# Optimization experiments

Measured on AMD Instinct MI355X. Metric: run time of the kernel, lower is better.

Reference implementation:

```python
import jax, jax.numpy as jnp
import numpy as np

N = 100000
E = 1600000
IN_C = 128
HID = 256
EPS = 1e-5


def setup_inputs() -> dict:
    key = jax.random.key(0)
    ks = jax.random.split(key, 20)
    s = lambda fi, fo: (1.0 / np.sqrt(fi))
    inp = {
        "x": jax.random.normal(ks[0], (N, IN_C), dtype=jnp.float32),
        "edge_index": jax.random.randint(ks[1], (2, E), 0, N, dtype=jnp.int64),
        # SAGEConv (in -> hidden): lin_l (on aggregated neighbors, with bias), lin_r (root, no bias)
        "Wl": jax.random.normal(ks[2], (HID, IN_C), dtype=jnp.float32) * s(IN_C, HID),
        "bl": jnp.zeros((HID,), dtype=jnp.float32),
        "Wr": jax.random.normal(ks[3], (HID, IN_C), dtype=jnp.float32) * s(IN_C, HID),
        # bns[0]
        "bn_g": jnp.ones((HID,), dtype=jnp.float32),
        "bn_b": jnp.zeros((HID,), dtype=jnp.float32),
        # linear stack hidden->hidden->64->14->2
        "W1": jax.random.normal(ks[4], (HID, HID), dtype=jnp.float32) * s(HID, HID),
        "b1": jnp.zeros((HID,), dtype=jnp.float32),
        "W2": jax.random.normal(ks[5], (64, HID), dtype=jnp.float32) * s(HID, 64),
        "b2": jnp.zeros((64,), dtype=jnp.float32),
        "W3": jax.random.normal(ks[6], (14, 64), dtype=jnp.float32) * s(64, 14),
        "b3": jnp.zeros((14,), dtype=jnp.float32),
        "W4": jax.random.normal(ks[7], (2, 14), dtype=jnp.float32) * s(14, 2),
        "b4": jnp.zeros((2,), dtype=jnp.float32),
        # bns2: BN(hidden), BN(64), BN(14)
        "g1": jnp.ones((HID,), dtype=jnp.float32), "bb1": jnp.zeros((HID,), dtype=jnp.float32),
        "g2": jnp.ones((64,), dtype=jnp.float32), "bb2": jnp.zeros((64,), dtype=jnp.float32),
        "g3": jnp.ones((14,), dtype=jnp.float32), "bb3": jnp.zeros((14,), dtype=jnp.float32),
    }
    return inp


def _bn(h, g, b):
    # training-mode BatchNorm1d: batch mean, biased variance
    m = h.mean(axis=0)
    v = jnp.mean((h - m) ** 2, axis=0)
    return g * (h - m) * jax.lax.rsqrt(v + EPS) + b


def _sage_mean(x, edge_index, Wl, bl, Wr):
    src, dst = edge_index[0], edge_index[1]
    n = x.shape[0]
    agg = jax.ops.segment_sum(x[src], dst, num_segments=n)  # [N, F]
    cnt = jax.ops.segment_sum(jnp.ones((src.shape[0],), x.dtype), dst, num_segments=n)
    agg = agg / jnp.maximum(cnt, 1.0)[:, None]
    return agg @ Wl.T + bl + x @ Wr.T


def reference(x, edge_index, Wl, bl, Wr, bn_g, bn_b,
              W1, b1, W2, b2, W3, b3, W4, b4,
              g1, bb1, g2, bb2, g3, bb3):
    # convs2[:-1] loop (num_layers=2 -> single conv), dropout is identity (eval)
    h = _sage_mean(x, edge_index, Wl, bl, Wr)
    h = jax.nn.relu(_bn(h, bn_g, bn_b))
    # linear stack with bns2 + relu
    h = jax.nn.relu(_bn(h @ W1.T + b1, g1, bb1))
    h = jax.nn.relu(_bn(h @ W2.T + b2, g2, bb2))
    h = jax.nn.relu(_bn(h @ W3.T + b3, g3, bb3))
    h = h @ W4.T + b4
    return jax.nn.log_softmax(h, axis=-1)
```

## Files before the change

### kernel.cpp

```cpp
#include <hip/hip_runtime.h>
#include <math.h>

#define BN_EPS 1e-5f
#define STAT_NB 64
#define GBIN 512
#define BSH 7

typedef unsigned short u16;
typedef __attribute__((ext_vector_type(8))) unsigned short u16x8;
typedef __attribute__((ext_vector_type(8))) short bf16x8;
typedef __attribute__((ext_vector_type(4))) float f32x4;

__device__ __forceinline__ float bf2f(u16 b){
  union{unsigned int u; float f;} c; c.u = ((unsigned int)b)<<16; return c.f;
}
__device__ __forceinline__ u16 f2bf(float f){
  union{float f; unsigned int u;} c; c.f=f;
  unsigned int u = c.u;
  return (u16)((u + 0x7fffu + ((u>>16)&1u)) >> 16);
}

__global__ __launch_bounds__(256) void k_prep(
    const float* __restrict__ Wl, const float* __restrict__ Wr,
    const float* __restrict__ W1, const float* __restrict__ W2,
    const float* __restrict__ x,
    u16* __restrict__ Wb1, u16* __restrict__ Wb2, u16* __restrict__ Wb3,
    u16* __restrict__ Acat, int n, int* __restrict__ flags){
  int bid = blockIdx.x, tid = threadIdx.x;
  if (bid==0 && tid<8) flags[tid]=0;
  auto cv8 = [](const float* s)->u16x8{
    float4 a = ((const float4*)s)[0], b = ((const float4*)s)[1];
    u16x8 v;
    v[0]=f2bf(a.x); v[1]=f2bf(a.y); v[2]=f2bf(a.z); v[3]=f2bf(a.w);
    v[4]=f2bf(b.x); v[5]=f2bf(b.y); v[6]=f2bf(b.z); v[7]=f2bf(b.w);
    return v;
  };
  if (bid < 32){
    int i = bid*256 + tid;
    int c = i>>5, kb = (i&31)*8;
    const float* src = (kb<128) ? (Wl + (size_t)c*128 + kb) : (Wr + (size_t)c*128 + kb-128);
    *(u16x8*)(Wb1 + (size_t)c*256 + kb) = cv8(src);
  } else if (bid < 64){
    int i = (bid-32)*256 + tid;
    *(u16x8*)(Wb2 + (size_t)i*8) = cv8(W1 + (size_t)i*8);
  } else if (bid < 72){
    int i = (bid-64)*256 + tid;
    if (i < 2048) *(u16x8*)(Wb3 + (size_t)i*8) = cv8(W2 + (size_t)i*8);
  } else {
    int i = (bid-72)*256 + tid;
    int total = n*16;
    int stride = (gridDim.x-72)*256;
    for (; i<total; i+=stride){
      int r = i>>4, kb = (i&15)*8;
      *(u16x8*)(Acat + (size_t)r*256 + 128 + kb) = cv8(x + (size_t)r*128 + kb);
    }
  }
}


__global__ __launch_bounds__(256) void k_hist(const int* __restrict__ ei, int E, int nbkt,
                                              int* __restrict__ blkhist){
  __shared__ int hist[1024];
  int tid = threadIdx.x, blk = blockIdx.x;
  for (int b=tid;b<1024;b+=256) hist[b]=0;
  __syncthreads();
  int per = (E + GBIN - 1)/GBIN;
  int e0 = blk*per, e1 = min(E, e0+per);
  for (int e=e0+tid; e<e1; e+=256)
    atomicAdd(&hist[ei[(size_t)E+e]>>BSH], 1);
  __syncthreads();
  for (int b=tid;b<nbkt;b+=256) blkhist[(size_t)b*GBIN + blk] = hist[b];
}

__global__ __launch_bounds__(256) void k_rowscan(int* __restrict__ blkhist, int nbkt,
                                                 int* __restrict__ bbase){
  int wid = (blockIdx.x*blockDim.x + threadIdx.x) >> 6;
  int lane = threadIdx.x & 63;
  if (wid >= nbkt) return;
  int* row = blkhist + (size_t)wid*GBIN + lane*8;
  int v[8];
  #pragma unroll
  for (int j=0;j<8;j++) v[j] = row[j];
  int s = 0;
  #pragma unroll
  for (int j=0;j<8;j++){ int t = v[j]; v[j] = s; s += t; }
  int incl = s;
  #pragma unroll
  for (int o=1;o<64;o<<=1){
    int t = __shfl_up(incl, o, 64);
    if (lane >= o) incl += t;
  }
  int excl = incl - s;
  #pragma unroll
  for (int j=0;j<8;j++) row[j] = v[j] + excl;
  if (lane == 63) bbase[wid] = incl;
}

__global__ void k_bscan(int* __restrict__ bbase, int nbkt){
  __shared__ int s[1024];
  int tid = threadIdx.x;
  int v = (tid<nbkt)? bbase[tid] : 0;
  s[tid]=v; __syncthreads();
  #pragma unroll
  for (int o=1;o<1024;o<<=1){
    int t = (tid>=o)? s[tid-o] : 0;
    __syncthreads();
    s[tid]+=t;
    __syncthreads();
  }
  if (tid<nbkt) bbase[tid] = s[tid]-v;
  if (tid==1023) bbase[nbkt] = s[1023];
}

__global__ __launch_bounds__(256) void k_scatter(const int* __restrict__ ei, int E, int nbkt,
                                                 const int* __restrict__ blkhist,
                                                 const int* __restrict__ bbase,
                                                 int* __restrict__ pairs){
  __shared__ int cur[1024];
  int tid = threadIdx.x, blk = blockIdx.x;
  for (int b=tid;b<nbkt;b+=256) cur[b] = bbase[b] + blkhist[(size_t)b*GBIN + blk];
  __syncthreads();
  int per = (E + GBIN - 1)/GBIN;
  int e0 = blk*per, e1 = min(E, e0+per);
  for (int e=e0+tid; e<e1; e+=256){
    int dst = ei[(size_t)E+e];
    int src = ei[e];
    int b = dst>>BSH;
    int p = atomicAdd(&cur[b], 1);
    pairs[p] = (src<<BSH) | (dst & 127);
  }
}

__global__ __launch_bounds__(256) void k_bucket_csr(const int* __restrict__ pairs,
                                                    const int* __restrict__ bbase,
                                                    int nbkt, int n,
                                                    int* __restrict__ deg, int* __restrict__ off,
                                                    int* __restrict__ eidx){
  __shared__ int hist[128], loff[128], cur2[128];
  int tid = threadIdx.x, b = blockIdx.x;
  if (b >= nbkt) return;
  int n0 = b<<BSH;
  int nn = min(128, n - n0);
  int e0 = bbase[b], e1 = bbase[b+1];
  int cnt = e1 - e0;
  if (tid<128) hist[tid]=0;
  __syncthreads();
  for (int i=tid;i<cnt;i+=256)
    atomicAdd(&hist[pairs[e0+i] & 127], 1);
  __syncthreads();
  int hv=0;
  if (tid<128){ hv = hist[tid]; loff[tid] = hv; }
  __syncthreads();
  #pragma unroll
  for (int o=1;o<128;o<<=1){
    int t = (tid<128 && tid>=o)? loff[tid-o] : 0;
    __syncthreads();
    if (tid<128) loff[tid]+=t;
    __syncthreads();
  }
  if (tid<128){
    int ex = loff[tid]-hv;
    cur2[tid] = ex;
    if (tid<nn){
      deg[n0+tid] = hv;
      off[n0+tid] = e0 + ex;
    }
  }
  __syncthreads();
  for (int i=tid;i<cnt;i+=256){
    int v = pairs[e0+i];
    int p = atomicAdd(&cur2[v & 127], 1);
    eidx[e0 + p] = v>>BSH;
  }
}

__global__ void k_aggregate(u16* Acat, const int* __restrict__ off,
                            const int* __restrict__ deg, const int* __restrict__ eidx, int n){
  int wid = (blockIdx.x*blockDim.x + threadIdx.x) >> 6;
  int lane = threadIdx.x & 63;
  if (wid >= n) return;
  int o = off[wid], d = deg[wid];
  int eslot = lane >> 3;
  int ck = (lane & 7) * 16;
  float f[16];
  #pragma unroll
  for (int j=0;j<16;j++) f[j]=0.f;
  #pragma unroll 2
  for (int i = eslot; i < d; i += 8){
    int s = eidx[o+i];
    const u16x8* src = (const u16x8*)(Acat + (size_t)s*256 + 128 + ck);
    u16x8 v0 = src[0], v1 = src[1];
    #pragma unroll
    for (int j=0;j<8;j++) f[j]   += bf2f(v0[j]);
    #pragma unroll
    for (int j=0;j<8;j++) f[8+j] += bf2f(v1[j]);
  }
  #pragma unroll
  for (int j=0;j<16;j++){
    f[j] += __shfl_xor(f[j], 8, 64);
    f[j] += __shfl_xor(f[j], 16, 64);
    f[j] += __shfl_xor(f[j], 32, 64);
  }
  if (lane < 8){
    float inv = 1.f/(float)max(d,1);
    u16x8 r0, r1;
    #pragma unroll
    for (int j=0;j<8;j++){ r0[j]=f2bf(f[j]*inv); r1[j]=f2bf(f[8+j]*inv); }
    u16x8* dst = (u16x8*)(Acat + (size_t)wid*256 + ck);
    dst[0]=r0; dst[1]=r1;
  }
}


template<int COLS>
__global__ __launch_bounds__(256, 2) void k_gemm_mfma(
    const u16* __restrict__ A, const u16* __restrict__ W,
    const float* __restrict__ ss, int has_ss,
    const float* __restrict__ bias, u16* __restrict__ out,
    int nrows, int hout,
    float* __restrict__ psum, float* __restrict__ psq)
{
  constexpr int WN  = COLS/2;
  constexpr int NFR = WN/16;
  __shared__ u16 As[128*64];
  __shared__ u16 Bs[COLS*64];
  __shared__ float scs[256], shs[256];
  __shared__ float red[2][2][COLS];

  int tid  = threadIdx.x;
  int lane = tid & 63, wave = tid >> 6;
  int wr = wave >> 1, wc = wave & 1;
  int rbase = blockIdx.x*128;
  constexpr int cbase = 0;

  if (has_ss){ scs[tid] = ss[tid]; shs[tid] = ss[256+tid]; }
  __syncthreads();

  f32x4 acc[4][NFR];
  #pragma unroll
  for (int m=0;m<4;m++)
    #pragma unroll
    for (int n=0;n<NFR;n++)
      acc[m][n] = (f32x4){0.f,0.f,0.f,0.f};

  int arow = tid >> 1;
  int acb  = (tid & 1) * 32;
  bool avalid = (rbase + arow) < nrows;
  const u16* aptr = A + (size_t)(rbase+arow)*256 + acb;
  int brow, bcb;
  if (COLS==256)      { brow = tid;    bcb = 0; }
  else if (COLS==128) { brow = tid>>1; bcb = (tid&1)*32; }
  else                { brow = tid>>2; bcb = (tid&3)*16; }
  const u16* bptr = W + (size_t)(cbase+brow)*256 + bcb;

  for (int kt=0; kt<256; kt+=64){
    #pragma unroll
    for (int q=0;q<4;q++){
      u16x8 v = (u16x8){0,0,0,0,0,0,0,0};
      if (avalid) v = *(const u16x8*)(aptr + kt + q*8);
      if (has_ss){
        int k = acb + q*8;
        #pragma unroll
        for (int e=0;e<8;e++){
          float f = bf2f(v[e]);
          f = fmaxf(fmaf(f, scs[kt+k+e], shs[kt+k+e]), 0.f);
          v[e] = f2bf(f);
        }
      }
      int slot = ((acb>>3) + q) ^ (arow & 7);
      *(u16x8*)(As + arow*64 + slot*8) = v;
    }
    #pragma unroll
    for (int q=0;q<(COLS==256?8:COLS/32);q++){
      u16x8 v = *(const u16x8*)(bptr + kt + q*8);
      int slot = ((bcb>>3) + q) ^ (brow & 7);
      *(u16x8*)(Bs + brow*64 + slot*8) = v;
    }
    __syncthreads();

    int fr = lane & 15, g = lane >> 4;
    #pragma unroll
    for (int kk=0;kk<2;kk++){
      bf16x8 af[4], bfr[NFR];
      #pragma unroll
      for (int m=0;m<4;m++){
        int row = wr*64 + m*16 + fr;
        int slot = (kk*4 + g) ^ (row & 7);
        af[m] = *(const bf16x8*)(As + row*64 + slot*8);
      }
      #pragma unroll
      for (int n=0;n<NFR;n++){
        int row = wc*WN + n*16 + fr;
        int slot = (kk*4 + g) ^ (row & 7);
        bfr[n] = *(const bf16x8*)(Bs + row*64 + slot*8);
      }
      #pragma unroll
      for (int m=0;m<4;m++)
        #pragma unroll
        for (int n=0;n<NFR;n++)
          acc[m][n] = __builtin_amdgcn_mfma_f32_16x16x32_bf16(af[m], bfr[n], acc[m][n], 0, 0, 0);
    }
    __syncthreads();
  }

  int cl = lane & 15, g = lane >> 4;
  float bv[NFR], sn[NFR], qn[NFR];
  #pragma unroll
  for (int n=0;n<NFR;n++){
    bv[n] = bias[cbase + wc*WN + n*16 + cl];
    sn[n] = 0.f; qn[n] = 0.f;
  }
  #pragma unroll
  for (int m=0;m<4;m++){
    int r0 = rbase + wr*64 + m*16 + g*4;
    #pragma unroll
    for (int n=0;n<NFR;n++){
      int c = cbase + wc*WN + n*16 + cl;
      #pragma unroll
      for (int i=0;i<4;i++){
        int r = r0 + i;
        if (r < nrows){
          float v = acc[m][n][i] + bv[n];
          out[(size_t)r*hout + c] = f2bf(v);
          sn[n] += v; qn[n] += v*v;
        }
      }
    }
  }
  #pragma unroll
  for (int n=0;n<NFR;n++){
    sn[n] += __shfl_xor(sn[n], 16, 64);
    sn[n] += __shfl_xor(sn[n], 32, 64);
    qn[n] += __shfl_xor(qn[n], 16, 64);
    qn[n] += __shfl_xor(qn[n], 32, 64);
  }
  if (lane < 16){
    #pragma unroll
    for (int n=0;n<NFR;n++){
      int cc = wc*WN + n*16 + lane;
      red[0][wr][cc] = sn[n];
      red[1][wr][cc] = qn[n];
    }
  }
  __syncthreads();
  if (tid < COLS){
    psum[(size_t)blockIdx.x*hout + cbase + tid] = red[0][0][tid] + red[0][1][tid];
    psq [(size_t)blockIdx.x*hout + cbase + tid] = red[1][0][tid] + red[1][1][tid];
  }
}

__global__ __launch_bounds__(256) void k_stats_partfold(
    const float* __restrict__ psum, const float* __restrict__ psq,
    int rt, int h, float* __restrict__ part, float ninv,
    const float* __restrict__ g, const float* __restrict__ b_,
    float* __restrict__ ss, int* __restrict__ counter){
  __shared__ int isLast;
  int c = threadIdx.x, b = blockIdx.x;
  int chunk = (rt + STAT_NB - 1)/STAT_NB;
  int i0 = b*chunk;
  int i1 = min(rt, i0+chunk);
  if (c < h){
    float s0=0.f,s1=0.f,s2=0.f,s3=0.f, q0=0.f,q1=0.f,q2=0.f,q3=0.f;
    int i=i0;
    for (; i+3<i1; i+=4){
      s0 += psum[(size_t)i*h+c];     q0 += psq[(size_t)i*h+c];
      s1 += psum[(size_t)(i+1)*h+c]; q1 += psq[(size_t)(i+1)*h+c];
      s2 += psum[(size_t)(i+2)*h+c]; q2 += psq[(size_t)(i+2)*h+c];
      s3 += psum[(size_t)(i+3)*h+c]; q3 += psq[(size_t)(i+3)*h+c];
    }
    for (; i<i1; ++i){ s0 += psum[(size_t)i*h+c]; q0 += psq[(size_t)i*h+c]; }
    part[((size_t)b*2  )*h + c] = (s0+s1)+(s2+s3);
    part[((size_t)b*2+1)*h + c] = (q0+q1)+(q2+q3);
  }
  __threadfence();
  if (c==0) isLast = (atomicAdd(counter,1) == gridDim.x-1);
  __syncthreads();
  if (isLast && c < h){
    float S0=0.f,S1=0.f,Q0=0.f,Q1=0.f;
    #pragma unroll 2
    for (int b2=0;b2<STAT_NB;b2+=2){
      S0 += part[((size_t)b2*2  )*h + c];
      Q0 += part[((size_t)b2*2+1)*h + c];
      S1 += part[((size_t)(b2+1)*2  )*h + c];
      Q1 += part[((size_t)(b2+1)*2+1)*h + c];
    }
    float S = S0+S1, Q = Q0+Q1;
    float m = S*ninv;
    float v = fmaxf(Q*ninv - m*m, 0.f);
    float sc = g[c] * rsqrtf(v + BN_EPS);
    ss[c]   = sc;
    ss[h+c] = b_[c] - m*sc;
  }
}

__global__ __launch_bounds__(256) void k_lin3(const u16* __restrict__ h3, const float* __restrict__ ss3,
     const float* __restrict__ W3, const float* __restrict__ b3,
     float* __restrict__ h4, int n, float* __restrict__ psum, float* __restrict__ psq){
  __shared__ float Ws[14*64];
  __shared__ float bs[14];
  __shared__ float sc[64], sh[64];
  __shared__ float redp[2][14][4];
  int tid=threadIdx.x;
  for (int i=tid;i<896;i+=256) Ws[i]=W3[i];
  if (tid<14) bs[tid]=b3[tid];
  if (tid<64){ sc[tid]=ss3[tid]; sh[tid]=ss3[64+tid]; }
  __syncthreads();
  int node = blockIdx.x*256 + tid;
  float o[14];
  #pragma unroll
  for (int hh=0;hh<14;hh++) o[hh]=0.f;
  if (node<n){
    const u16x8* ar = (const u16x8*)(h3 + (size_t)node*64);
    #pragma unroll
    for (int kv=0;kv<8;kv++){
      u16x8 v = ar[kv];
      #pragma unroll
      for (int j=0;j<8;j++){
        int k=kv*8+j;
        float a = fmaxf(fmaf(bf2f(v[j]), sc[k], sh[k]), 0.f);
        #pragma unroll
        for (int hh=0;hh<14;hh++) o[hh] = fmaf(a, Ws[hh*64+k], o[hh]);
      }
    }
    #pragma unroll
    for (int hh=0;hh<14;hh++){ o[hh]+=bs[hh]; h4[(size_t)node*14+hh]=o[hh]; }
  }
  int lane = tid & 63, w = tid>>6;
  #pragma unroll
  for (int hh=0;hh<14;hh++){
    float sv = (node<n)? o[hh] : 0.f;
    float qv = sv*sv;
    #pragma unroll
    for (int offs=32;offs>0;offs>>=1){
      sv += __shfl_down(sv,offs,64);
      qv += __shfl_down(qv,offs,64);
    }
    if (lane==0){ redp[0][hh][w]=sv; redp[1][hh][w]=qv; }
  }
  __syncthreads();
  if (tid<14){
    float t=redp[0][tid][0]+redp[0][tid][1]+redp[0][tid][2]+redp[0][tid][3];
    psum[(size_t)blockIdx.x*14+tid]=t;
  } else if (tid>=64 && tid<78){
    int c=tid-64;
    float t=redp[1][c][0]+redp[1][c][1]+redp[1][c][2]+redp[1][c][3];
    psq[(size_t)blockIdx.x*14+c]=t;
  }
}

__global__ void k_final(const float* __restrict__ h4, const float* __restrict__ ss4,
   const float* __restrict__ W4, const float* __restrict__ b4, float* __restrict__ out, int n){
  int node = blockIdx.x*blockDim.x+threadIdx.x;
  if (node>=n) return;
  float z0=b4[0], z1=b4[1];
  #pragma unroll
  for (int j=0;j<14;j++){
    float a = fmaxf(h4[(size_t)node*14+j]*ss4[j]+ss4[14+j], 0.f);
    z0 = fmaf(a, W4[j],    z0);
    z1 = fmaf(a, W4[14+j], z1);
  }
  float m = fmaxf(z0,z1);
  float lse = m + logf(expf(z0-m)+expf(z1-m));
  out[(size_t)node*2]   = z0-lse;
  out[(size_t)node*2+1] = z1-lse;
}

extern "C" void kernel_launch(void* const* d_in, const int* in_sizes, int n_in,
                              void* d_out, int out_size, void* d_ws, size_t ws_size,
                              hipStream_t stream){
  const float* x    = (const float*)d_in[0];
  const int*   ei   = (const int*)d_in[1];
  const float* Wl   = (const float*)d_in[2];
  const float* bl   = (const float*)d_in[3];
  const float* Wr   = (const float*)d_in[4];
  const float* bn_g = (const float*)d_in[5];
  const float* bn_b = (const float*)d_in[6];
  const float* W1   = (const float*)d_in[7];
  const float* b1   = (const float*)d_in[8];
  const float* W2   = (const float*)d_in[9];
  const float* b2   = (const float*)d_in[10];
  const float* W3   = (const float*)d_in[11];
  const float* b3   = (const float*)d_in[12];
  const float* W4   = (const float*)d_in[13];
  const float* b4   = (const float*)d_in[14];
  const float* g1   = (const float*)d_in[15];
  const float* bb1  = (const float*)d_in[16];
  const float* g2   = (const float*)d_in[17];
  const float* bb2  = (const float*)d_in[18];
  const float* g3   = (const float*)d_in[19];
  const float* bb3  = (const float*)d_in[20];

  const int N = in_sizes[0]/128;
  const int E = in_sizes[1]/2;
  const int NBKT = (N + 127) >> BSH;
  const int RT2 = (N+127)/128;
  const int RT4 = (N+255)/256;

  char* p = (char*)d_ws;
  auto alloc = [&](size_t bytes)->void*{
    void* r = (void*)p;
    p += (bytes + 255) & ~(size_t)255;
    return r;
  };
  int* deg      = (int*)alloc((size_t)N*sizeof(int));
  int* off      = (int*)alloc((size_t)N*sizeof(int));
  int* bbase    = (int*)alloc(1025*sizeof(int));
  int* flags    = (int*)alloc(16*sizeof(int));
  int* blkhist  = (int*)alloc((size_t)1024*GBIN*sizeof(int));
  int* pairs    = (int*)alloc((size_t)E*sizeof(int));
  int* eidx     = (int*)alloc((size_t)E*sizeof(int));
  u16* Acat     = (u16*)alloc((size_t)N*256*sizeof(u16));
  u16* h1b      = (u16*)alloc((size_t)N*256*sizeof(u16));
  float* h4     = (float*)alloc((size_t)N*14*sizeof(float));
  u16* Wb1      = (u16*)alloc(256*256*sizeof(u16));
  u16* Wb2      = (u16*)alloc(256*256*sizeof(u16));
  u16* Wb3      = (u16*)alloc(64*256*sizeof(u16));
  float* psum   = (float*)alloc((size_t)RT2*256*sizeof(float));
  float* psq    = (float*)alloc((size_t)RT2*256*sizeof(float));
  float* part   = (float*)alloc((size_t)STAT_NB*2*256*sizeof(float));
  float* ssb    = (float*)alloc(4*512*sizeof(float));
  u16* h2b = Acat;
  u16* h3b = h1b;
  float* ss1=ssb, *ss2=ssb+512, *ss3=ssb+1024, *ss4=ssb+1536;
  const float ninv = 1.f/(float)N;

  k_prep<<<dim3(72+2048), dim3(256), 0, stream>>>(Wl, Wr, W1, W2, x, Wb1, Wb2, Wb3, Acat, N, flags);

  k_hist<<<dim3(GBIN), dim3(256), 0, stream>>>(ei, E, NBKT, blkhist);
  k_rowscan<<<dim3((NBKT*64+255)/256), dim3(256), 0, stream>>>(blkhist, NBKT, bbase);
  k_bscan<<<dim3(1), dim3(1024), 0, stream>>>(bbase, NBKT);
  k_scatter<<<dim3(GBIN), dim3(256), 0, stream>>>(ei, E, NBKT, blkhist, bbase, pairs);
  k_bucket_csr<<<dim3(NBKT), dim3(256), 0, stream>>>(pairs, bbase, NBKT, N, deg, off, eidx);

  k_aggregate<<<dim3((N+3)/4), dim3(256), 0, stream>>>(Acat, off, deg, eidx, N);

  k_gemm_mfma<256><<<dim3(RT2), dim3(256), 0, stream>>>(
      Acat, Wb1, (const float*)0, 0, bl, h1b, N, 256, psum, psq);
  k_stats_partfold<<<dim3(STAT_NB), dim3(256), 0, stream>>>(
      psum, psq, RT2, 256, part, ninv, bn_g, bn_b, ss1, flags+0);

  k_gemm_mfma<256><<<dim3(RT2), dim3(256), 0, stream>>>(
      h1b, Wb2, ss1, 1, b1, h2b, N, 256, psum, psq);
  k_stats_partfold<<<dim3(STAT_NB), dim3(256), 0, stream>>>(
      psum, psq, RT2, 256, part, ninv, g1, bb1, ss2, flags+1);

  k_gemm_mfma<64><<<dim3(RT2), dim3(256), 0, stream>>>(
      h2b, Wb3, ss2, 1, b2, h3b, N, 64, psum, psq);
  k_stats_partfold<<<dim3(STAT_NB), dim3(256), 0, stream>>>(
      psum, psq, RT2, 64, part, ninv, g2, bb2, ss3, flags+2);

  k_lin3<<<dim3(RT4), dim3(256), 0, stream>>>(h3b, ss3, W3, b3, h4, N, psum, psq);
  k_stats_partfold<<<dim3(STAT_NB), dim3(256), 0, stream>>>(
      psum, psq, RT4, 14, part, ninv, g3, bb3, ss4, flags+3);

  k_final<<<dim3((N+255)/256), dim3(256), 0, stream>>>(h4, ss4, W4, b4, (float*)d_out, N);
}
```

Before: 302.0 us.

## Fuse histogram into prep, merge scans, use direct-to-LDS loads in GEMM

Folds the edge histogram into the prep kernel and merges the bucket-base scan into the row scan using a last-block counter, which removes two kernel launches. Packs offset and degree into one int2 array so the aggregate kernel does a single load per node. Replaces the register-staged tile loads in the MFMA GEMM with global_load_lds for the weights and for the un-normalized A operand, and raises occupancy for the 64-column variant. The last-block counter depends on the flags being zeroed by the prep kernel before the row scan starts. The direct-to-LDS A path has no bounds check on the final partial row tile.

```diff
diff --git a/kernel.cpp b/kernel.cpp
--- a/kernel.cpp
+++ b/kernel.cpp
@@ -5,6 +5,7 @@
 #define STAT_NB 64
 #define GBIN 512
 #define BSH 7
+#define XB 2048
 
 typedef unsigned short u16;
 typedef __attribute__((ext_vector_type(8))) unsigned short u16x8;
@@ -19,15 +20,19 @@
   unsigned int u = c.u;
   return (u16)((u + 0x7fffu + ((u>>16)&1u)) >> 16);
 }
+__device__ __forceinline__ void gl16(const u16* g, u16* l){
+  __builtin_amdgcn_global_load_lds((const __attribute__((address_space(1))) void*)g,
+                                   (__attribute__((address_space(3))) void*)l, 16, 0, 0);
+}
 
 __global__ __launch_bounds__(256) void k_prep(
     const float* __restrict__ Wl, const float* __restrict__ Wr,
     const float* __restrict__ W1, const float* __restrict__ W2,
-    const float* __restrict__ x,
+    const float* __restrict__ x, const int* __restrict__ ei, int E, int nbkt,
     u16* __restrict__ Wb1, u16* __restrict__ Wb2, u16* __restrict__ Wb3,
-    u16* __restrict__ Acat, int n, int* __restrict__ flags){
+    u16* __restrict__ Acat, int n, int* __restrict__ blkhist, int* __restrict__ flags){
+  __shared__ int hist[1024];
   int bid = blockIdx.x, tid = threadIdx.x;
-  if (bid==0 && tid<8) flags[tid]=0;
   auto cv8 = [](const float* s)->u16x8{
     float4 a = ((const float4*)s)[0], b = ((const float4*)s)[1];
     u16x8 v;
@@ -35,81 +40,92 @@
     v[4]=f2bf(b.x); v[5]=f2bf(b.y); v[6]=f2bf(b.z); v[7]=f2bf(b.w);
     return v;
   };
-  if (bid < 32){
+  if (bid < XB){
     int i = bid*256 + tid;
-    int c = i>>5, kb = (i&31)*8;
-    const float* src = (kb<128) ? (Wl + (size_t)c*128 + kb) : (Wr + (size_t)c*128 + kb-128);
-    *(u16x8*)(Wb1 + (size_t)c*256 + kb) = cv8(src);
-  } else if (bid < 64){
-    int i = (bid-32)*256 + tid;
-    *(u16x8*)(Wb2 + (size_t)i*8) = cv8(W1 + (size_t)i*8);
-  } else if (bid < 72){
-    int i = (bid-64)*256 + tid;
-    if (i < 2048) *(u16x8*)(Wb3 + (size_t)i*8) = cv8(W2 + (size_t)i*8);
-  } else {
-    int i = (bid-72)*256 + tid;
     int total = n*16;
-    int stride = (gridDim.x-72)*256;
-    for (; i<total; i+=stride){
+    for (; i<total; i+=XB*256){
       int r = i>>4, kb = (i&15)*8;
       *(u16x8*)(Acat + (size_t)r*256 + 128 + kb) = cv8(x + (size_t)r*128 + kb);
     }
-  }
-}
-
-
-__global__ __launch_bounds__(256) void k_hist(const int* __restrict__ ei, int E, int nbkt,
-                                              int* __restrict__ blkhist){
-  __shared__ int hist[1024];
-  int tid = threadIdx.x, blk = blockIdx.x;
-  for (int b=tid;b<1024;b+=256) hist[b]=0;
-  __syncthreads();
-  int per = (E + GBIN - 1)/GBIN;
-  int e0 = blk*per, e1 = min(E, e0+per);
-  for (int e=e0+tid; e<e1; e+=256)
-    atomicAdd(&hist[ei[(size_t)E+e]>>BSH], 1);
-  __syncthreads();
-  for (int b=tid;b<nbkt;b+=256) blkhist[(size_t)b*GBIN + blk] = hist[b];
+  } else if (bid < XB+512){
+    int blk = bid - XB;
+    for (int b=tid;b<1024;b+=256) hist[b]=0;
+    __syncthreads();
+    int per = (E + GBIN - 1)/GBIN;
+    int e0 = blk*per, e1 = min(E, e0+per);
+    for (int e=e0+tid; e<e1; e+=256)
+      atomicAdd(&hist[ei[(size_t)E+e]>>BSH], 1);
+    __syncthreads();
+    for (int b=tid;b<nbkt;b+=256) blkhist[(size_t)b*GBIN + blk] = hist[b];
+  } else {
+    int wb = bid - (XB+512);
+    if (wb==0 && tid<8) flags[tid]=0;
+    if (wb < 32){
+      int i = wb*256 + tid;
+      int c = i>>5, kb = (i&31)*8;
+      const float* src = (kb<128) ? (Wl + (size_t)c*128 + kb) : (Wr + (size_t)c*128 + kb-128);
+      *(u16x8*)(Wb1 + (size_t)c*256 + kb) = cv8(src);
+    } else if (wb < 64){
+      int i = (wb-32)*256 + tid;
+      *(u16x8*)(Wb2 + (size_t)i*8) = cv8(W1 + (size_t)i*8);
+    } else {
+      int i = (wb-64)*256 + tid;
+      if (i < 2048) *(u16x8*)(Wb3 + (size_t)i*8) = cv8(W2 + (size_t)i*8);
+    }
+  }
 }
 
 __global__ __launch_bounds__(256) void k_rowscan(int* __restrict__ blkhist, int nbkt,
-                                                 int* __restrict__ bbase){
-  int wid = (blockIdx.x*blockDim.x + threadIdx.x) >> 6;
-  int lane = threadIdx.x & 63;
-  if (wid >= nbkt) return;
-  int* row = blkhist + (size_t)wid*GBIN + lane*8;
-  int v[8];
-  #pragma unroll
-  for (int j=0;j<8;j++) v[j] = row[j];
-  int s = 0;
-  #pragma unroll
-  for (int j=0;j<8;j++){ int t = v[j]; v[j] = s; s += t; }
-  int incl = s;
-  #pragma unroll
-  for (int o=1;o<64;o<<=1){
-    int t = __shfl_up(incl, o, 64);
-    if (lane >= o) incl += t;
-  }
-  int excl = incl - s;
-  #pragma unroll
-  for (int j=0;j<8;j++) row[j] = v[j] + excl;
-  if (lane == 63) bbase[wid] = incl;
-}
-
-__global__ void k_bscan(int* __restrict__ bbase, int nbkt){
-  __shared__ int s[1024];
+                                                 int* __restrict__ bbase, int* __restrict__ counter){
+  __shared__ int lastFlag;
+  __shared__ int ps[256];
   int tid = threadIdx.x;
-  int v = (tid<nbkt)? bbase[tid] : 0;
-  s[tid]=v; __syncthreads();
-  #pragma unroll
-  for (int o=1;o<1024;o<<=1){
-    int t = (tid>=o)? s[tid-o] : 0;
-    __syncthreads();
-    s[tid]+=t;
-    __syncthreads();
-  }
-  if (tid<nbkt) bbase[tid] = s[tid]-v;
-  if (tid==1023) bbase[nbkt] = s[1023];
+  int wid = (blockIdx.x*256 + tid) >> 6;
+  int lane = tid & 63;
+  if (wid < nbkt){
+    int* row = blkhist + (size_t)wid*GBIN + lane*8;
+    int v[8];
+    #pragma unroll
+    for (int j=0;j<8;j++) v[j] = row[j];
+    int s = 0;
+    #pragma unroll
+    for (int j=0;j<8;j++){ int t = v[j]; v[j] = s; s += t; }
+    int incl = s;
+    #pragma unroll
+    for (int o=1;o<64;o<<=1){
+      int t = __shfl_up(incl, o, 64);
+      if (lane >= o) incl += t;
+    }
+    int excl = incl - s;
+    #pragma unroll
+    for (int j=0;j<8;j++) row[j] = v[j] + excl;
+    if (lane == 63) bbase[wid] = incl;
+  }
+  __threadfence();
+  if (tid==0) lastFlag = (atomicAdd(counter,1) == (int)gridDim.x-1);
+  __syncthreads();
+  if (!lastFlag) return;
+  int base = tid*4;
+  int v0 = (base  <nbkt)? bbase[base  ] : 0;
+  int v1 = (base+1<nbkt)? bbase[base+1] : 0;
+  int v2 = (base+2<nbkt)? bbase[base+2] : 0;
+  int v3 = (base+3<nbkt)? bbase[base+3] : 0;
+  int run = v0+v1+v2+v3;
+  ps[tid] = run;
+  __syncthreads();
+  #pragma unroll
+  for (int o=1;o<256;o<<=1){
+    int t = (tid>=o)? ps[tid-o] : 0;
+    __syncthreads();
+    ps[tid] += t;
+    __syncthreads();
+  }
+  int excl = ps[tid]-run;
+  if (base  <nbkt) bbase[base  ] = excl;
+  if (base+1<nbkt) bbase[base+1] = excl+v0;
+  if (base+2<nbkt) bbase[base+2] = excl+v0+v1;
+  if (base+3<nbkt) bbase[base+3] = excl+v0+v1+v2;
+  if (tid==255) bbase[nbkt] = ps[255];
 }
 
 __global__ __launch_bounds__(256) void k_scatter(const int* __restrict__ ei, int E, int nbkt,
@@ -134,7 +150,7 @@
 __global__ __launch_bounds__(256) void k_bucket_csr(const int* __restrict__ pairs,
                                                     const int* __restrict__ bbase,
                                                     int nbkt, int n,
-                                                    int* __restrict__ deg, int* __restrict__ off,
+                                                    int2* __restrict__ odeg,
                                                     int* __restrict__ eidx){
   __shared__ int hist[128], loff[128], cur2[128];
   int tid = threadIdx.x, b = blockIdx.x;
@@ -161,10 +177,7 @@
   if (tid<128){
     int ex = loff[tid]-hv;
     cur2[tid] = ex;
-    if (tid<nn){
-      deg[n0+tid] = hv;
-      off[n0+tid] = e0 + ex;
-    }
+    if (tid<nn) odeg[n0+tid] = make_int2(e0+ex, hv);
   }
   __syncthreads();
   for (int i=tid;i<cnt;i+=256){
@@ -174,12 +187,13 @@
   }
 }
 
-__global__ void k_aggregate(u16* Acat, const int* __restrict__ off,
-                            const int* __restrict__ deg, const int* __restrict__ eidx, int n){
+__global__ void k_aggregate(u16* Acat, const int2* __restrict__ odeg,
+                            const int* __restrict__ eidx, int n){
   int wid = (blockIdx.x*blockDim.x + threadIdx.x) >> 6;
   int lane = threadIdx.x & 63;
   if (wid >= n) return;
-  int o = off[wid], d = deg[wid];
+  int2 od = odeg[wid];
+  int o = od.x, d = od.y;
   int eslot = lane >> 3;
   int ck = (lane & 7) * 16;
   float f[16];
@@ -213,7 +227,7 @@
 
 
 template<int COLS>
-__global__ __launch_bounds__(256, 2) void k_gemm_mfma(
+__global__ __launch_bounds__(256, COLS==64?4:2) void k_gemm_mfma(
     const u16* __restrict__ A, const u16* __restrict__ W,
     const float* __restrict__ ss, int has_ss,
     const float* __restrict__ bias, u16* __restrict__ out,
@@ -222,6 +236,7 @@
 {
   constexpr int WN  = COLS/2;
   constexpr int NFR = WN/16;
+  constexpr int BC  = (COLS*8)/256;
   __shared__ u16 As[128*64];
   __shared__ u16 Bs[COLS*64];
   __shared__ float scs[256], shs[256];
@@ -231,7 +246,6 @@
   int lane = tid & 63, wave = tid >> 6;
   int wr = wave >> 1, wc = wave & 1;
   int rbase = blockIdx.x*128;
-  constexpr int cbase = 0;
 
   if (has_ss){ scs[tid] = ss[tid]; shs[tid] = ss[256+tid]; }
   __syncthreads();
@@ -247,18 +261,13 @@
   int acb  = (tid & 1) * 32;
   bool avalid = (rbase + arow) < nrows;
   const u16* aptr = A + (size_t)(rbase+arow)*256 + acb;
-  int brow, bcb;
-  if (COLS==256)      { brow = tid;    bcb = 0; }
-  else if (COLS==128) { brow = tid>>1; bcb = (tid&1)*32; }
-  else                { brow = tid>>2; bcb = (tid&3)*16; }
-  const u16* bptr = W + (size_t)(cbase+brow)*256 + bcb;
 
   for (int kt=0; kt<256; kt+=64){
-    #pragma unroll
-    for (int q=0;q<4;q++){
-      u16x8 v = (u16x8){0,0,0,0,0,0,0,0};
-      if (avalid) v = *(const u16x8*)(aptr + kt + q*8);
-      if (has_ss){
+    if (has_ss){
+      #pragma unroll
+      for (int q=0;q<4;q++){
+        u16x8 v = (u16x8){0,0,0,0,0,0,0,0};
+        if (avalid) v = *(const u16x8*)(aptr + kt + q*8);
         int k = acb + q*8;
         #pragma unroll
         for (int e=0;e<8;e++){
@@ -266,15 +275,26 @@
           f = fmaxf(fmaf(f, scs[kt+k+e], shs[kt+k+e]), 0.f);
           v[e] = f2bf(f);
         }
+        int slot = ((acb>>3) + q) ^ (arow & 7);
+        *(u16x8*)(As + arow*64 + slot*8) = v;
       }
-      int slot = ((acb>>3) + q) ^ (arow & 7);
-      *(u16x8*)(As + arow*64 + slot*8) = v;
-    }
-    #pragma unroll
-    for (int q=0;q<(COLS==256?8:COLS/32);q++){
-      u16x8 v = *(const u16x8*)(bptr + kt + q*8);
-      int slot = ((bcb>>3) + q) ^ (brow & 7);
-      *(u16x8*)(Bs + brow*64 + slot*8) = v;
+    } else {
+      #pragma unroll
+      for (int q=0;q<4;q++){
+        int cb = (wave*4+q)*64;
+        int c = cb + lane;
+        int row = c>>3, sl = c&7;
+        const u16* g = A + (size_t)(rbase+row)*256 + kt + ((sl ^ (row&7))<<3);
+        gl16(g, As + cb*8);
+      }
+    }
+    #pragma unroll
+    for (int q=0;q<BC;q++){
+      int cb = (wave*BC+q)*64;
+      int c = cb + lane;
+      int row = c>>3, sl = c&7;
+      const u16* g = W + (size_t)row*256 + kt + ((sl ^ (row&7))<<3);
+      gl16(g, Bs + cb*8);
     }
     __syncthreads();
 
@@ -307,7 +327,7 @@
   float bv[NFR], sn[NFR], qn[NFR];
   #pragma unroll
   for (int n=0;n<NFR;n++){
-    bv[n] = bias[cbase + wc*WN + n*16 + cl];
+    bv[n] = bias[wc*WN + n*16 + cl];
     sn[n] = 0.f; qn[n] = 0.f;
   }
   #pragma unroll
@@ -315,7 +335,7 @@
     int r0 = rbase + wr*64 + m*16 + g*4;
     #pragma unroll
     for (int n=0;n<NFR;n++){
-      int c = cbase + wc*WN + n*16 + cl;
+      int c = wc*WN + n*16 + cl;
       #pragma unroll
       for (int i=0;i<4;i++){
         int r = r0 + i;
@@ -344,8 +364,8 @@
   }
   __syncthreads();
   if (tid < COLS){
-    psum[(size_t)blockIdx.x*hout + cbase + tid] = red[0][0][tid] + red[0][1][tid];
-    psq [(size_t)blockIdx.x*hout + cbase + tid] = red[1][0][tid] + red[1][1][tid];
+    psum[(size_t)blockIdx.x*hout + tid] = red[0][0][tid] + red[0][1][tid];
+    psq [(size_t)blockIdx.x*hout + tid] = red[1][0][tid] + red[1][1][tid];
   }
 }
 
@@ -502,8 +522,7 @@
     p += (bytes + 255) & ~(size_t)255;
     return r;
   };
-  int* deg      = (int*)alloc((size_t)N*sizeof(int));
-  int* off      = (int*)alloc((size_t)N*sizeof(int));
+  int2* odeg    = (int2*)alloc((size_t)N*sizeof(int2));
   int* bbase    = (int*)alloc(1025*sizeof(int));
   int* flags    = (int*)alloc(16*sizeof(int));
   int* blkhist  = (int*)alloc((size_t)1024*GBIN*sizeof(int));
@@ -524,15 +543,14 @@
   float* ss1=ssb, *ss2=ssb+512, *ss3=ssb+1024, *ss4=ssb+1536;
   const float ninv = 1.f/(float)N;
 
-  k_prep<<<dim3(72+2048), dim3(256), 0, stream>>>(Wl, Wr, W1, W2, x, Wb1, Wb2, Wb3, Acat, N, flags);
-
-  k_hist<<<dim3(GBIN), dim3(256), 0, stream>>>(ei, E, NBKT, blkhist);
-  k_rowscan<<<dim3((NBKT*64+255)/256), dim3(256), 0, stream>>>(blkhist, NBKT, bbase);
-  k_bscan<<<dim3(1), dim3(1024), 0, stream>>>(bbase, NBKT);
+  k_prep<<<dim3(XB+512+72), dim3(256), 0, stream>>>(
+      Wl, Wr, W1, W2, x, ei, E, NBKT, Wb1, Wb2, Wb3, Acat, N, blkhist, flags);
+
+  k_rowscan<<<dim3((NBKT*64+255)/256), dim3(256), 0, stream>>>(blkhist, NBKT, bbase, flags+4);
   k_scatter<<<dim3(GBIN), dim3(256), 0, stream>>>(ei, E, NBKT, blkhist, bbase, pairs);
-  k_bucket_csr<<<dim3(NBKT), dim3(256), 0, stream>>>(pairs, bbase, NBKT, N, deg, off, eidx);
-
-  k_aggregate<<<dim3((N+3)/4), dim3(256), 0, stream>>>(Acat, off, deg, eidx, N);
+  k_bucket_csr<<<dim3(NBKT), dim3(256), 0, stream>>>(pairs, bbase, NBKT, N, odeg, eidx);
+
+  k_aggregate<<<dim3((N+3)/4), dim3(256), 0, stream>>>(Acat, odeg, eidx, N);
 
   k_gemm_mfma<256><<<dim3(RT2), dim3(256), 0, stream>>>(
       Acat, Wb1, (const float*)0, 0, bl, h1b, N, 256, psum, psq);
```

Result: no change. 306.1 us, median of 2 (+1.4%).
